# Kernel tuning notes

Hardware: AMD Instinct MI355X
Metric: run time of the kernel (lower is better)

Reference implementation:

```python
import jax, jax.numpy as jnp
import numpy as np


def setup_inputs() -> dict:
    key = jax.random.key(0)
    k1, k2 = jax.random.split(key)
    B, F, D = 4096, 32, 64
    P = F * (F - 1) // 2  # 496
    inputs = jax.random.normal(k1, (B, F, D), dtype=jnp.float32)
    W = jax.random.normal(k2, (P, D, D), dtype=jnp.float32) * 0.05
    return {"inputs": inputs, "W": W}


def reference(inputs, W):
    # inputs: (B, F, D); W: (P, D, D) with P = F*(F-1)/2 pairs in
    # itertools.combinations order (== np.triu_indices row-major order).
    F = inputs.shape[1]
    idx_i, idx_j = np.triu_indices(F, k=1)  # static pair indices
    vi = inputs[:, idx_i, :]                 # (B, P, D)
    vj = inputs[:, idx_j, :]                 # (B, P, D)
    # per-pair matmul v_i @ W_p, then elementwise multiply with v_j
    vidots = jnp.einsum('bpd,pde->bpe', vi, W)
    return vidots * vj                       # (B, P, D)
```

## Files before the change

### kernel.cpp

```cpp
#include <hip/hip_runtime.h>

#define Bsz 4096
#define Fsz 32
#define Dsz 64
#define Psz 496
#define BT  128
#define VIP 65

__global__ __launch_bounds__(256)
void bilinear_fp32_kernel(const float* __restrict__ in,
                          const float* __restrict__ W,
                          float* __restrict__ out) {
    __shared__ float sW[Dsz][Dsz];
    __shared__ float sVi[BT][VIP];

    const int p   = blockIdx.x;
    const int b0  = blockIdx.y * BT;
    const int tid = threadIdx.x;

    int i = 0, rem = p;
    while (rem >= Fsz - 1 - i) { rem -= Fsz - 1 - i; ++i; }
    const int j = i + 1 + rem;

    {
        const float4* gW  = (const float4*)(W + (size_t)p * Dsz * Dsz);
        float4*       sWv = (float4*)(&sW[0][0]);
#pragma unroll
        for (int k = 0; k < 4; ++k) sWv[tid + k * 256] = gW[tid + k * 256];
    }

    {
        const int rowq = tid >> 4;
        const int q    = tid & 15;
#pragma unroll
        for (int pass = 0; pass < BT / 16; ++pass) {
            const int r = pass * 16 + rowq;
            const float4 v = *(const float4*)(in + ((size_t)(b0 + r) * Fsz + i) * Dsz + q * 4);
            sVi[r][q * 4 + 0] = v.x;
            sVi[r][q * 4 + 1] = v.y;
            sVi[r][q * 4 + 2] = v.z;
            sVi[r][q * 4 + 3] = v.w;
        }
    }

    __syncthreads();

    const int tx  = tid & 7;
    const int ty  = tid >> 3;
    const int e0  = tx * 8;
    const int bl0 = ty * 4;

    float acc[4][8];
#pragma unroll
    for (int bb = 0; bb < 4; ++bb)
#pragma unroll
        for (int ee = 0; ee < 8; ++ee) acc[bb][ee] = 0.0f;

#pragma unroll 8
    for (int d = 0; d < Dsz; ++d) {
        float w[8];
        *(float4*)&w[0] = *(const float4*)&sW[d][e0];
        *(float4*)&w[4] = *(const float4*)&sW[d][e0 + 4];
        float v[4];
#pragma unroll
        for (int bb = 0; bb < 4; ++bb) v[bb] = sVi[bl0 + bb][d];
#pragma unroll
        for (int bb = 0; bb < 4; ++bb)
#pragma unroll
            for (int ee = 0; ee < 8; ++ee)
                acc[bb][ee] = fmaf(v[bb], w[ee], acc[bb][ee]);
    }

#pragma unroll
    for (int bb = 0; bb < 4; ++bb) {
        const size_t b   = (size_t)(b0 + bl0 + bb);
        const float* vjp = in + (b * Fsz + j) * Dsz + e0;
        const float4 vja = *(const float4*)(vjp);
        const float4 vjb = *(const float4*)(vjp + 4);
        float4 o0, o1;
        o0.x = acc[bb][0] * vja.x;
        o0.y = acc[bb][1] * vja.y;
        o0.z = acc[bb][2] * vja.z;
        o0.w = acc[bb][3] * vja.w;
        o1.x = acc[bb][4] * vjb.x;
        o1.y = acc[bb][5] * vjb.y;
        o1.z = acc[bb][6] * vjb.z;
        o1.w = acc[bb][7] * vjb.w;
        float* op = out + (b * Psz + p) * Dsz + e0;
        *(float4*)(op)     = o0;
        *(float4*)(op + 4) = o1;
    }
}

extern "C" void kernel_launch(void* const* d_in, const int* in_sizes, int n_in,
                              void* d_out, int out_size, void* d_ws, size_t ws_size,
                              hipStream_t stream) {
    const float* in  = (const float*)d_in[0];
    const float* W   = (const float*)d_in[1];
    float*       out = (float*)d_out;

    dim3 grid(Psz, Bsz / BT);
    bilinear_fp32_kernel<<<grid, 256, 0, stream>>>(in, W, out);
}
```

Before: 650.8 us.

## Hold each W column in registers and stream batch rows per wavefront

Replaces the shared-memory tiled matmul with a scheme where each lane keeps one full column of W_p (64 floats) in registers. Each wavefront then loops over 64 batch rows, loading v_i through wave-uniform scalar addresses and writing the output with nontemporal stores. This removes LDS traffic and __syncthreads, but it adds heavy register pressure (w and s arrays of 64 each) and a strided W load. The serial r loop also has no per-row data reuse beyond W.

```diff
diff --git a/kernel.cpp b/kernel.cpp
--- a/kernel.cpp
+++ b/kernel.cpp
@@ -4,91 +4,50 @@
 #define Fsz 32
 #define Dsz 64
 #define Psz 496
-#define BT  128
-#define VIP 65
+#define RPW 64
+#define WPB 4
 
 __global__ __launch_bounds__(256)
-void bilinear_fp32_kernel(const float* __restrict__ in,
+void bilinear_wreg_kernel(const float* __restrict__ in,
                           const float* __restrict__ W,
-                          float* __restrict__ out) {
-    __shared__ float sW[Dsz][Dsz];
-    __shared__ float sVi[BT][VIP];
+                          float* __restrict__ out)
+{
+    const int p    = blockIdx.x;
+    const int tid  = threadIdx.x;
+    const int lane = tid & 63;
 
-    const int p   = blockIdx.x;
-    const int b0  = blockIdx.y * BT;
-    const int tid = threadIdx.x;
+    const int bb0 = __builtin_amdgcn_readfirstlane(
+                        blockIdx.y * (RPW * WPB) + (tid >> 6) * RPW);
 
     int i = 0, rem = p;
     while (rem >= Fsz - 1 - i) { rem -= Fsz - 1 - i; ++i; }
     const int j = i + 1 + rem;
 
+    float w[Dsz];
     {
-        const float4* gW  = (const float4*)(W + (size_t)p * Dsz * Dsz);
-        float4*       sWv = (float4*)(&sW[0][0]);
+        const float* Wp = W + (size_t)p * (Dsz * Dsz) + lane;
 #pragma unroll
-        for (int k = 0; k < 4; ++k) sWv[tid + k * 256] = gW[tid + k * 256];
+        for (int d = 0; d < Dsz; ++d) w[d] = Wp[(size_t)d * Dsz];
     }
 
-    {
-        const int rowq = tid >> 4;
-        const int q    = tid & 15;
+    const float* __restrict__ vi0 = in  + ((size_t)bb0 * Fsz + i) * Dsz;
+    const float* __restrict__ vj0 = in  + ((size_t)bb0 * Fsz + j) * Dsz + lane;
+    float*       __restrict__ op0 = out + ((size_t)bb0 * Psz + p) * Dsz + lane;
+
+#pragma unroll 1
+    for (int r = 0; r < RPW; ++r) {
+        const float* vi  = vi0 + (size_t)r * (Fsz * Dsz);
+        const float  vjv = vj0[(size_t)r * (Fsz * Dsz)];
+
+        float s[Dsz];
 #pragma unroll
-        for (int pass = 0; pass < BT / 16; ++pass) {
-            const int r = pass * 16 + rowq;
-            const float4 v = *(const float4*)(in + ((size_t)(b0 + r) * Fsz + i) * Dsz + q * 4);
-            sVi[r][q * 4 + 0] = v.x;
-            sVi[r][q * 4 + 1] = v.y;
-            sVi[r][q * 4 + 2] = v.z;
-            sVi[r][q * 4 + 3] = v.w;
-        }
-    }
+        for (int d = 0; d < Dsz; ++d) s[d] = vi[d];
 
-    __syncthreads();
+        float acc = 0.0f;
+#pragma unroll
+        for (int d = 0; d < Dsz; ++d) acc = fmaf(s[d], w[d], acc);
 
-    const int tx  = tid & 7;
-    const int ty  = tid >> 3;
-    const int e0  = tx * 8;
-    const int bl0 = ty * 4;
-
-    float acc[4][8];
-#pragma unroll
-    for (int bb = 0; bb < 4; ++bb)
-#pragma unroll
-        for (int ee = 0; ee < 8; ++ee) acc[bb][ee] = 0.0f;
-
-#pragma unroll 8
-    for (int d = 0; d < Dsz; ++d) {
-        float w[8];
-        *(float4*)&w[0] = *(const float4*)&sW[d][e0];
-        *(float4*)&w[4] = *(const float4*)&sW[d][e0 + 4];
-        float v[4];
-#pragma unroll
-        for (int bb = 0; bb < 4; ++bb) v[bb] = sVi[bl0 + bb][d];
-#pragma unroll
-        for (int bb = 0; bb < 4; ++bb)
-#pragma unroll
-            for (int ee = 0; ee < 8; ++ee)
-                acc[bb][ee] = fmaf(v[bb], w[ee], acc[bb][ee]);
-    }
-
-#pragma unroll
-    for (int bb = 0; bb < 4; ++bb) {
-        const size_t b   = (size_t)(b0 + bl0 + bb);
-        const float* vjp = in + (b * Fsz + j) * Dsz + e0;
-        const float4 vja = *(const float4*)(vjp);
-        const float4 vjb = *(const float4*)(vjp + 4);
-        float4 o0, o1;
-        o0.x = acc[bb][0] * vja.x;
-        o0.y = acc[bb][1] * vja.y;
-        o0.z = acc[bb][2] * vja.z;
-        o0.w = acc[bb][3] * vja.w;
-        o1.x = acc[bb][4] * vjb.x;
-        o1.y = acc[bb][5] * vjb.y;
-        o1.z = acc[bb][6] * vjb.z;
-        o1.w = acc[bb][7] * vjb.w;
-        float* op = out + (b * Psz + p) * Dsz + e0;
-        *(float4*)(op)     = o0;
-        *(float4*)(op + 4) = o1;
+        __builtin_nontemporal_store(acc * vjv, op0 + (size_t)r * (Psz * Dsz));
     }
 }
 
@@ -99,6 +58,6 @@
     const float* W   = (const float*)d_in[1];
     float*       out = (float*)d_out;
 
-    dim3 grid(Psz, Bsz / BT);
-    bilinear_fp32_kernel<<<grid, 256, 0, stream>>>(in, W, out);
+    dim3 grid(Psz, Bsz / (RPW * WPB));
+    bilinear_wreg_kernel<<<grid, 256, 0, stream>>>(in, W, out);
 }
```

Measured after the change: 746.2 us. +14.7%, slower.
